# Optimization experiments

Hardware: AMD Instinct MI355X
Metric: run time of the kernel (lower is better)

Reference implementation:

```python
import jax, jax.numpy as jnp
import numpy as np

D_MODEL = 1024
NUM_HEADS = 16
D_K = D_MODEL // NUM_HEADS


def setup_inputs() -> dict:
    key = jax.random.key(0)
    k_x, k_q, k_k, k_v, k_o = jax.random.split(key, 5)
    s = 1.0 / np.sqrt(D_MODEL)
    return {
        "x": jax.random.normal(k_x, (2, 2048, D_MODEL), dtype=jnp.float32),
        "W_q": jax.random.normal(k_q, (D_MODEL, D_MODEL), dtype=jnp.float32) * s,
        "W_k": jax.random.normal(k_k, (D_MODEL, D_MODEL), dtype=jnp.float32) * s,
        "W_v": jax.random.normal(k_v, (D_MODEL, D_MODEL), dtype=jnp.float32) * s,
        "W_o": jax.random.normal(k_o, (D_MODEL, D_MODEL), dtype=jnp.float32) * s,
    }


def reference(x, W_q, W_k, W_v, W_o):
    B, S, D = x.shape
    H, dk = NUM_HEADS, D_K
    # nn.Linear(y) = y @ W.T ; weights stored as (out, in)
    def proj(W):
        return (x @ W.T).reshape(B, S, H, dk).transpose(0, 2, 1, 3)  # (B,H,S,dk)
    Q, K, V = proj(W_q), proj(W_k), proj(W_v)
    scores = jnp.einsum("bhqd,bhkd->bhqk", Q, K) / np.sqrt(dk)  # (B,H,S,S)
    attn = jax.nn.softmax(scores, axis=-1)
    out = jnp.einsum("bhqk,bhkd->bhqd", attn, V)  # (B,H,S,dk)
    out = out.transpose(0, 2, 1, 3).reshape(B, S, D)
    return out @ W_o.T
```

## Files before the change

### kernel.cpp

```cpp
#include <hip/hip_runtime.h>
#include <hip/hip_bf16.h>

#define SEQ 2048
#define DM  1024
#define NH  16
#define DK  64
#define MROWS 4096

typedef __attribute__((ext_vector_type(8))) short short8;
typedef __attribute__((ext_vector_type(4))) short short4v;
typedef __attribute__((ext_vector_type(4))) float float4v;
typedef __attribute__((ext_vector_type(2))) unsigned uint2v;

typedef const __attribute__((address_space(1))) unsigned gu32;
typedef __attribute__((address_space(3))) unsigned lu32;

__device__ __forceinline__ void gl2lds16(const void* g, void* l) {
  __builtin_amdgcn_global_load_lds((gu32*)g, (lu32*)l, 16, 0, 0);
}

__device__ __forceinline__ short f2bf(float f) {
  union { float f; unsigned u; } v; v.f = f;
  unsigned r = v.u + 0x7fffu + ((v.u >> 16) & 1u);
  return (short)(r >> 16);
}

#if __has_builtin(__builtin_amdgcn_exp2f)
#define EXP2(x) __builtin_amdgcn_exp2f(x)
#else
#define EXP2(x) exp2f(x)
#endif

__device__ __forceinline__ unsigned pack_bfu(float a, float b) {
  unsigned ua = __float_as_uint(a) + 0x8000u;
  unsigned ub = __float_as_uint(b) + 0x8000u;
#if __has_builtin(__builtin_amdgcn_perm)
  return __builtin_amdgcn_perm(ub, ua, 0x07060302u);
#else
  return (ua >> 16) | (ub & 0xffff0000u);
#endif
}

__global__ __launch_bounds__(256) void cvt_kernel(
    const float* __restrict__ in, short* __restrict__ out) {
  int i = blockIdx.x * 256 + threadIdx.x;
  float4v f = ((const float4v*)in)[i];
  short4v s;
#pragma unroll
  for (int j = 0; j < 4; ++j) s[j] = f2bf(f[j]);
  ((short4v*)out)[i] = s;
}

__global__ __launch_bounds__(256) void cvt4_kernel(
    const float* __restrict__ a, const float* __restrict__ b,
    const float* __restrict__ c, const float* __restrict__ d,
    short* __restrict__ out) {
  const float* srcs[4] = {a, b, c, d};
  const float* s = srcs[blockIdx.y];
  int i = blockIdx.x * 256 + threadIdx.x;
  float4v f = ((const float4v*)s)[i];
  short4v sv;
#pragma unroll
  for (int j = 0; j < 4; ++j) sv[j] = f2bf(f[j]);
  ((short4v*)(out + (size_t)blockIdx.y * DM * DM))[i] = sv;
}

template<int TM, int TN, int MINW, typename TC>
__global__ __launch_bounds__(256, MINW) void gemm_bt(
    const short* __restrict__ A, const short* __restrict__ Bw0,
    TC* __restrict__ C0, int M, int N, int K, size_t strB, size_t strC,
    short* __restrict__ vtOut, float qs0)
{
  constexpr int NI = TN / 32;
  constexpr int CA = TM * 64 / (8 * 256);
  constexpr int CB = TN * 64 / (8 * 256);
  constexpr int STG = (TM + TN) * 64;
  constexpr int TSZ = TN * 72;
  constexpr int SM_SZ = (TN == 128 && TSZ > STG) ? TSZ : STG;
  __shared__ __align__(16) short SMEM[SM_SZ];
  short* Al = SMEM;
  short* Bl = SMEM + TM * 64;

  const short* Bw = Bw0 + (size_t)blockIdx.z * strB;
  TC* C = C0 + (size_t)blockIdx.z * strC;

  const int tid  = threadIdx.x;
  const int lane = tid & 63, wave = tid >> 6;
  const int l16  = lane & 15, quad = lane >> 4;
  const int wm   = (wave >> 1) * 32, wn = (wave & 1) * (TN / 2);
  const int cm   = blockIdx.y * TM, cn = blockIdx.x * TN;

  float4v acc[2][NI];
#pragma unroll
  for (int i = 0; i < 2; ++i)
#pragma unroll
    for (int j = 0; j < NI; ++j)
#pragma unroll
      for (int r = 0; r < 4; ++r) acc[i][j][r] = 0.f;

  const short* ag = A  + (size_t)cm * K;
  const short* bg = Bw + (size_t)cn * K;

  auto stage = [&](int k0) {
#pragma unroll
    for (int i = 0; i < CA; ++i) {
      int c = i * 256 + tid;
      int row = c >> 3, cg = (c & 7) ^ (row & 7);
      gl2lds16(ag + (size_t)row * K + k0 + cg * 8, &Al[(i * 4 + wave) * 512]);
    }
#pragma unroll
    for (int i = 0; i < CB; ++i) {
      int c = i * 256 + tid;
      int row = c >> 3, cg = (c & 7) ^ (row & 7);
      gl2lds16(bg + (size_t)row * K + k0 + cg * 8, &Bl[(i * 4 + wave) * 512]);
    }
  };
  auto compute = [&]() {
#pragma unroll
    for (int ks = 0; ks < 2; ++ks) {
      const int sw = ((ks * 4 + quad) ^ (l16 & 7)) << 3;
      short8 af[2], bfr[NI];
#pragma unroll
      for (int mi = 0; mi < 2; ++mi)
        af[mi] = *(const short8*)&Al[(wm + mi*16 + l16) * 64 + sw];
#pragma unroll
      for (int ni = 0; ni < NI; ++ni)
        bfr[ni] = *(const short8*)&Bl[(wn + ni*16 + l16) * 64 + sw];
#pragma unroll
      for (int mi = 0; mi < 2; ++mi)
#pragma unroll
        for (int ni = 0; ni < NI; ++ni)
          acc[mi][ni] = __builtin_amdgcn_mfma_f32_16x16x32_bf16(
              af[mi], bfr[ni], acc[mi][ni], 0, 0, 0);
    }
  };

  for (int k0 = 0; k0 < K; k0 += 64) {
    stage(k0);
    __syncthreads();
    compute();
    __syncthreads();
  }

  const float scl = (blockIdx.z == 0) ? qs0 : 1.f;

  if constexpr (TN == 128) {
    if (vtOut != nullptr && blockIdx.z == 2) {
      short* T = SMEM;
#pragma unroll
      for (int mi = 0; mi < 2; ++mi)
#pragma unroll
        for (int ni = 0; ni < NI; ++ni)
#pragma unroll
          for (int r = 0; r < 4; ++r)
            T[(wn + ni*16 + l16) * 72 + wm + mi*16 + quad*4 + r] =
                f2bf(acc[mi][ni][r]);
      __syncthreads();
      const int nrow = tid >> 1, mo = (tid & 1) * 32;
      const int b = cm >> 11;
      const int s0 = (cm & (SEQ - 1)) + mo;
      short* vt = vtOut + ((size_t)b * DM + cn + nrow) * SEQ + s0;
#pragma unroll
      for (int j = 0; j < 4; ++j)
        *(short8*)(vt + j * 8) = *(const short8*)&T[nrow * 72 + mo + j * 8];
      return;
    }
  }
#pragma unroll
  for (int mi = 0; mi < 2; ++mi)
#pragma unroll
    for (int ni = 0; ni < NI; ++ni)
#pragma unroll
      for (int r = 0; r < 4; ++r) {
        int m = cm + wm + mi*16 + quad*4 + r;
        int n = cn + wn + ni*16 + l16;
        float v = acc[mi][ni][r] * scl;
        if constexpr (sizeof(TC) == 2) C[(size_t)m * N + n] = f2bf(v);
        else                           C[(size_t)m * N + n] = v;
      }
}

__global__ __launch_bounds__(512, 4) void flash_kernel(
    const short* __restrict__ Q, const short* __restrict__ Kg,
    const short* __restrict__ VTg, short* __restrict__ AO)
{
  __shared__ __align__(16) short Kl[2][64 * 64];
  __shared__ __align__(16) short Vt[2][64 * 64];
  __shared__ __align__(16) short Pl[8][16 * 64];
  __shared__ float lsumL[8][16];
  const int tid  = threadIdx.x;
  const int lane = tid & 63, wave = tid >> 6;
  const int l16  = lane & 15, quad = lane >> 4;
  const int hc   = blockIdx.x * DK;
  const int q0   = blockIdx.y * 128;
  const size_t base = (size_t)blockIdx.z * SEQ;

  short8 qfr[2];
#pragma unroll
  for (int ks = 0; ks < 2; ++ks)
    qfr[ks] = *(const short8*)(Q + (base + q0 + wave*16 + l16) * DM
                               + hc + ks*32 + quad*8);

  float4v O[4];
  float lsum = 0.f;
#pragma unroll
  for (int nt = 0; nt < 4; ++nt)
#pragma unroll
    for (int r = 0; r < 4; ++r) O[nt][r] = 0.f;

  const float4v z4 = {0.f, 0.f, 0.f, 0.f};
  const short* vtb = VTg + ((size_t)blockIdx.z * DM + hc) * SEQ;

  auto stageKV = [&](int buf, int kb) {
    int row = tid >> 3, cg = (tid & 7) ^ (row & 7);
    gl2lds16(Kg + (base + kb*64 + row) * DM + hc + cg * 8, &Kl[buf][wave * 512]);
    gl2lds16(vtb + (size_t)row * SEQ + kb*64 + cg * 8, &Vt[buf][wave * 512]);
  };

  stageKV(0, 0);
  __syncthreads();

  int cur = 0;
  for (int kb = 0; kb < SEQ / 64; ++kb) {
    if (kb + 1 < SEQ / 64) stageKV(cur ^ 1, kb + 1);

    float4v s[4];
#pragma unroll
    for (int kf = 0; kf < 4; ++kf) {
      const int rowb = (kf*16 + l16) * 64;
      short8 k0 = *(const short8*)&Kl[cur][rowb + ((quad       ^ (l16 & 7)) << 3)];
      short8 k1 = *(const short8*)&Kl[cur][rowb + (((4 + quad) ^ (l16 & 7)) << 3)];
      float4v t = __builtin_amdgcn_mfma_f32_16x16x32_bf16(k0, qfr[0], z4, 0, 0, 0);
      s[kf]     = __builtin_amdgcn_mfma_f32_16x16x32_bf16(k1, qfr[1], t, 0, 0, 0);
    }
#pragma unroll
    for (int kf = 0; kf < 4; ++kf) {
      float p0 = EXP2(s[kf][0]), p1 = EXP2(s[kf][1]);
      float p2 = EXP2(s[kf][2]), p3 = EXP2(s[kf][3]);
      lsum += (p0 + p1) + (p2 + p3);
      uint2v pk;
      pk[0] = pack_bfu(p0, p1);
      pk[1] = pack_bfu(p2, p3);
      *(uint2v*)&Pl[wave][l16 * 64 +
                          ((kf*16 + quad*4) ^ ((l16 & 7) << 3))] = pk;
    }
#pragma unroll
    for (int ks = 0; ks < 2; ++ks) {
      const int sw = ((ks*4 + quad) ^ (l16 & 7)) << 3;
      short8 pf = *(const short8*)&Pl[wave][l16 * 64 + sw];
#pragma unroll
      for (int nt = 0; nt < 4; ++nt) {
        short8 vf = *(const short8*)&Vt[cur][(nt*16 + l16) * 64 + sw];
        O[nt] = __builtin_amdgcn_mfma_f32_16x16x32_bf16(pf, vf, O[nt], 0, 0, 0);
      }
    }
    __syncthreads();
    cur ^= 1;
  }

  {
    float l = lsum;
    l += __shfl_xor(l, 16, 64);
    l += __shfl_xor(l, 32, 64);
    lsumL[wave][l16] = l;
  }
  float inv[4];
#pragma unroll
  for (int r = 0; r < 4; ++r) inv[r] = 1.f / lsumL[wave][quad*4 + r];
#pragma unroll
  for (int nt = 0; nt < 4; ++nt)
#pragma unroll
    for (int r = 0; r < 4; ++r) {
      int m = q0 + wave*16 + quad*4 + r;
      AO[(base + m) * DM + hc + nt*16 + l16] = f2bf(O[nt][r] * inv[r]);
    }
}

extern "C" void kernel_launch(void* const* d_in, const int* in_sizes, int n_in,
                              void* d_out, int out_size, void* d_ws, size_t ws_size,
                              hipStream_t stream) {
  (void)in_sizes; (void)n_in; (void)out_size; (void)ws_size;
  const float* x  = (const float*)d_in[0];
  const float* Wq = (const float*)d_in[1];
  const float* Wk = (const float*)d_in[2];
  const float* Wv = (const float*)d_in[3];
  const float* Wo = (const float*)d_in[4];
  float* out = (float*)d_out;

  const size_t NX = (size_t)MROWS * DM;
  const size_t NW = (size_t)DM * DM;
  short* xb  = (short*)d_ws;
  short* Wqb = xb  + NX;
  short* Qb  = Wqb + 4 * NW;
  short* Kb  = Qb  + NX;
  short* AO  = Kb  + NX;
  short* VTb = AO  + NX;

  cvt_kernel<<<dim3(NX / 4 / 256), 256, 0, stream>>>(x, xb);
  cvt4_kernel<<<dim3(NW / 4 / 256, 4), 256, 0, stream>>>(Wq, Wk, Wv, Wo, Wqb);

  const float qs = 0.18033688011112042f;

  gemm_bt<64, 128, 6, short><<<dim3(DM / 128, MROWS / 64, 3), 256, 0, stream>>>(
      xb, Wqb, Qb, MROWS, DM, DM, NW, NX, VTb, qs);

  flash_kernel<<<dim3(NH, SEQ / 128, 2), 512, 0, stream>>>(Qb, Kb, VTb, AO);

  gemm_bt<64, 64, 6, float><<<dim3(DM / 64, MROWS / 64, 1), 256, 0, stream>>>(
      AO, Wqb + 3 * NW, out, MROWS, DM, DM, 0, 0, nullptr, 1.f);
}
```

Measured before the change: 187.6 us.

## Merge conversion kernels and retile GEMMs to two-wave blocks with larger per-wave tiles

Replaces the two fp32-to-bf16 conversion launches with a single kernel covering x and all four weights. The GEMM template is generalised over per-wave MFMA tile counts and wave grid. The QKV and output projections now run 128-thread blocks where each wave computes a larger tile (64x64 or 32x64), which raises register-level reuse. The grid is also swapped so consecutive blocks walk the M dimension. The trade-off is fewer waves per block and lower occupancy bounds, which could reduce latency hiding. The V-transpose epilogue is adjusted for the single wave-row layout.

```diff
diff --git a/kernel.cpp b/kernel.cpp
--- a/kernel.cpp
+++ b/kernel.cpp
@@ -41,42 +41,41 @@
 #endif
 }
 
-__global__ __launch_bounds__(256) void cvt_kernel(
-    const float* __restrict__ in, short* __restrict__ out) {
-  int i = blockIdx.x * 256 + threadIdx.x;
-  float4v f = ((const float4v*)in)[i];
-  short4v s;
-#pragma unroll
-  for (int j = 0; j < 4; ++j) s[j] = f2bf(f[j]);
-  ((short4v*)out)[i] = s;
-}
-
-__global__ __launch_bounds__(256) void cvt4_kernel(
-    const float* __restrict__ a, const float* __restrict__ b,
-    const float* __restrict__ c, const float* __restrict__ d,
-    short* __restrict__ out) {
-  const float* srcs[4] = {a, b, c, d};
-  const float* s = srcs[blockIdx.y];
-  int i = blockIdx.x * 256 + threadIdx.x;
-  float4v f = ((const float4v*)s)[i];
+__global__ __launch_bounds__(256) void cvt5_kernel(
+    const float* __restrict__ x,  const float* __restrict__ Wq,
+    const float* __restrict__ Wk, const float* __restrict__ Wv,
+    const float* __restrict__ Wo, short* __restrict__ xb,
+    short* __restrict__ wb) {
+  size_t c4 = (size_t)blockIdx.x * 256 + threadIdx.x;
+  const float* s; short* d; size_t off;
+  if (c4 < (1u << 20)) { s = x; d = xb; off = c4; }
+  else {
+    size_t j = c4 - (1u << 20);
+    int w = (int)(j >> 18);
+    off = j & ((1u << 18) - 1);
+    s = (w == 0) ? Wq : (w == 1) ? Wk : (w == 2) ? Wv : Wo;
+    d = wb + ((size_t)w << 20);
+  }
+  float4v f = ((const float4v*)s)[off];
   short4v sv;
 #pragma unroll
   for (int j = 0; j < 4; ++j) sv[j] = f2bf(f[j]);
-  ((short4v*)(out + (size_t)blockIdx.y * DM * DM))[i] = sv;
-}
-
-template<int TM, int TN, int MINW, typename TC>
-__global__ __launch_bounds__(256, MINW) void gemm_bt(
+  ((short4v*)d)[off] = sv;
+}
+
+template<int MI, int NI, int RW, int CW, int MINW, typename TC>
+__global__ __launch_bounds__(RW*CW*64, MINW) void gemm_bt(
     const short* __restrict__ A, const short* __restrict__ Bw0,
     TC* __restrict__ C0, int M, int N, int K, size_t strB, size_t strC,
     short* __restrict__ vtOut, float qs0)
 {
-  constexpr int NI = TN / 32;
-  constexpr int CA = TM * 64 / (8 * 256);
-  constexpr int CB = TN * 64 / (8 * 256);
+  constexpr int NWAVES = RW * CW, THREADS = NWAVES * 64;
+  constexpr int TM = MI * 16 * RW, TN = NI * 16 * CW;
+  constexpr int CA = TM * 64 / (8 * THREADS);
+  constexpr int CB = TN * 64 / (8 * THREADS);
   constexpr int STG = (TM + TN) * 64;
-  constexpr int TSZ = TN * 72;
-  constexpr int SM_SZ = (TN == 128 && TSZ > STG) ? TSZ : STG;
+  constexpr int TSZ = (RW == 1 && TN == 128) ? 128 * 72 : 0;
+  constexpr int SM_SZ = STG > TSZ ? STG : TSZ;
   __shared__ __align__(16) short SMEM[SM_SZ];
   short* Al = SMEM;
   short* Bl = SMEM + TM * 64;
@@ -87,12 +86,12 @@
   const int tid  = threadIdx.x;
   const int lane = tid & 63, wave = tid >> 6;
   const int l16  = lane & 15, quad = lane >> 4;
-  const int wm   = (wave >> 1) * 32, wn = (wave & 1) * (TN / 2);
-  const int cm   = blockIdx.y * TM, cn = blockIdx.x * TN;
-
-  float4v acc[2][NI];
-#pragma unroll
-  for (int i = 0; i < 2; ++i)
+  const int wm   = (wave / CW) * MI * 16, wn = (wave % CW) * NI * 16;
+  const int cm   = blockIdx.x * TM, cn = blockIdx.y * TN;
+
+  float4v acc[MI][NI];
+#pragma unroll
+  for (int i = 0; i < MI; ++i)
 #pragma unroll
     for (int j = 0; j < NI; ++j)
 #pragma unroll
@@ -104,30 +103,32 @@
   auto stage = [&](int k0) {
 #pragma unroll
     for (int i = 0; i < CA; ++i) {
-      int c = i * 256 + tid;
+      int c = i * THREADS + tid;
       int row = c >> 3, cg = (c & 7) ^ (row & 7);
-      gl2lds16(ag + (size_t)row * K + k0 + cg * 8, &Al[(i * 4 + wave) * 512]);
+      gl2lds16(ag + (size_t)row * K + k0 + cg * 8,
+               &Al[(i * NWAVES + wave) * 512]);
     }
 #pragma unroll
     for (int i = 0; i < CB; ++i) {
-      int c = i * 256 + tid;
+      int c = i * THREADS + tid;
       int row = c >> 3, cg = (c & 7) ^ (row & 7);
-      gl2lds16(bg + (size_t)row * K + k0 + cg * 8, &Bl[(i * 4 + wave) * 512]);
+      gl2lds16(bg + (size_t)row * K + k0 + cg * 8,
+               &Bl[(i * NWAVES + wave) * 512]);
     }
   };
   auto compute = [&]() {
 #pragma unroll
     for (int ks = 0; ks < 2; ++ks) {
       const int sw = ((ks * 4 + quad) ^ (l16 & 7)) << 3;
-      short8 af[2], bfr[NI];
-#pragma unroll
-      for (int mi = 0; mi < 2; ++mi)
+      short8 af[MI], bfr[NI];
+#pragma unroll
+      for (int mi = 0; mi < MI; ++mi)
         af[mi] = *(const short8*)&Al[(wm + mi*16 + l16) * 64 + sw];
 #pragma unroll
       for (int ni = 0; ni < NI; ++ni)
         bfr[ni] = *(const short8*)&Bl[(wn + ni*16 + l16) * 64 + sw];
 #pragma unroll
-      for (int mi = 0; mi < 2; ++mi)
+      for (int mi = 0; mi < MI; ++mi)
 #pragma unroll
         for (int ni = 0; ni < NI; ++ni)
           acc[mi][ni] = __builtin_amdgcn_mfma_f32_16x16x32_bf16(
@@ -144,30 +145,30 @@
 
   const float scl = (blockIdx.z == 0) ? qs0 : 1.f;
 
-  if constexpr (TN == 128) {
+  if constexpr (RW == 1 && TN == 128) {
     if (vtOut != nullptr && blockIdx.z == 2) {
       short* T = SMEM;
 #pragma unroll
-      for (int mi = 0; mi < 2; ++mi)
+      for (int mi = 0; mi < MI; ++mi)
 #pragma unroll
         for (int ni = 0; ni < NI; ++ni)
 #pragma unroll
           for (int r = 0; r < 4; ++r)
-            T[(wn + ni*16 + l16) * 72 + wm + mi*16 + quad*4 + r] =
+            T[(wn + ni*16 + l16) * 72 + mi*16 + quad*4 + r] =
                 f2bf(acc[mi][ni][r]);
       __syncthreads();
-      const int nrow = tid >> 1, mo = (tid & 1) * 32;
+      const int nrow = tid;
       const int b = cm >> 11;
-      const int s0 = (cm & (SEQ - 1)) + mo;
+      const int s0 = cm & (SEQ - 1);
       short* vt = vtOut + ((size_t)b * DM + cn + nrow) * SEQ + s0;
 #pragma unroll
-      for (int j = 0; j < 4; ++j)
-        *(short8*)(vt + j * 8) = *(const short8*)&T[nrow * 72 + mo + j * 8];
+      for (int j = 0; j < 8; ++j)
+        *(short8*)(vt + j * 8) = *(const short8*)&T[nrow * 72 + j * 8];
       return;
     }
   }
 #pragma unroll
-  for (int mi = 0; mi < 2; ++mi)
+  for (int mi = 0; mi < MI; ++mi)
 #pragma unroll
     for (int ni = 0; ni < NI; ++ni)
 #pragma unroll
@@ -296,16 +297,15 @@
   short* AO  = Kb  + NX;
   short* VTb = AO  + NX;
 
-  cvt_kernel<<<dim3(NX / 4 / 256), 256, 0, stream>>>(x, xb);
-  cvt4_kernel<<<dim3(NW / 4 / 256, 4), 256, 0, stream>>>(Wq, Wk, Wv, Wo, Wqb);
+  cvt5_kernel<<<dim3(8192), 256, 0, stream>>>(x, Wq, Wk, Wv, Wo, xb, Wqb);
 
   const float qs = 0.18033688011112042f;
 
-  gemm_bt<64, 128, 6, short><<<dim3(DM / 128, MROWS / 64, 3), 256, 0, stream>>>(
+  gemm_bt<4, 4, 1, 2, 3, short><<<dim3(MROWS / 64, DM / 128, 3), 128, 0, stream>>>(
       xb, Wqb, Qb, MROWS, DM, DM, NW, NX, VTb, qs);
 
   flash_kernel<<<dim3(NH, SEQ / 128, 2), 512, 0, stream>>>(Qb, Kb, VTb, AO);
 
-  gemm_bt<64, 64, 6, float><<<dim3(DM / 64, MROWS / 64, 1), 256, 0, stream>>>(
+  gemm_bt<2, 4, 2, 1, 2, float><<<dim3(MROWS / 64, DM / 64, 1), 128, 0, stream>>>(
       AO, Wqb + 3 * NW, out, MROWS, DM, DM, 0, 0, nullptr, 1.f);
 }
```

After: 181.5 us. 1.03x faster.
